# Kernel optimization log

Measured on AMD Instinct MI355X. Metric: run time of the kernel, lower is better.

## Reference

```python
import jax, jax.numpy as jnp
import numpy as np

N_NODES = 20000
DIM = 512
N_EDGES = 320000  # first N_NODES edges are self-loops so every node has a predecessor
EPS = 1e-7


def _logmap0(y):
    # Poincare ball (c=1) log map at origin: artanh(||y||) * y / ||y||
    n = jnp.linalg.norm(y, axis=-1, keepdims=True)
    nc = jnp.clip(n, EPS, 1.0 - 1e-6)
    return jnp.arctanh(nc) * y / nc


def _expmap0(v):
    # Poincare ball (c=1) exp map at origin: tanh(||v||) * v / ||v||
    n = jnp.linalg.norm(v, axis=-1, keepdims=True)
    nc = jnp.maximum(n, EPS)
    return jnp.tanh(nc) * v / nc


def setup_inputs() -> dict:
    key = jax.random.key(0)
    ks = jax.random.split(key, 9)
    x_raw = jax.random.normal(ks[0], (N_NODES, DIM), dtype=jnp.float32)
    nrm = jnp.linalg.norm(x_raw, axis=-1, keepdims=True)
    x = 0.7 * x_raw / (1.0 + nrm)  # strictly inside the unit ball

    rng = np.random.RandomState(0)
    src_rand = rng.randint(0, N_NODES, size=N_EDGES - N_NODES)
    dst_rand = rng.randint(0, N_NODES, size=N_EDGES - N_NODES)
    loop = np.arange(N_NODES)
    src = jnp.asarray(np.concatenate([loop, src_rand]), dtype=jnp.int32)
    dst = jnp.asarray(np.concatenate([loop, dst_rand]), dtype=jnp.int32)

    s = 1.0 / np.sqrt(DIM)
    Wq = jax.random.normal(ks[1], (DIM, DIM), jnp.float32) * s
    bq = jax.random.normal(ks[2], (DIM,), jnp.float32) * 0.01
    Wk = jax.random.normal(ks[3], (DIM, DIM), jnp.float32) * s
    bk = jax.random.normal(ks[4], (DIM,), jnp.float32) * 0.01
    Wv = jax.random.normal(ks[5], (DIM, DIM), jnp.float32) * s
    bv = jax.random.normal(ks[6], (DIM,), jnp.float32) * 0.01
    Wo = jax.random.normal(ks[7], (DIM, DIM), jnp.float32) * s
    bo = jax.random.normal(ks[8], (DIM,), jnp.float32) * 0.01
    return dict(x=x, src=src, dst=dst, Wq=Wq, bq=bq, Wk=Wk, bk=bk,
                Wv=Wv, bv=bv, Wo=Wo, bo=bo)


def reference(x, src, dst, Wq, bq, Wk, bk, Wv, bv, Wo, bo):
    n_nodes, d = x.shape
    scale = 1.0 / jnp.sqrt(jnp.asarray(d, x.dtype))

    t = _logmap0(x)                                  # [N, d] tangent vectors
    q = (t @ Wq.T + bq) * scale                      # torch MHA scales q
    k = t @ Wk.T + bk
    v = t @ Wv.T + bv

    # Per-destination attention over predecessor (src) neighbors.
    scores = jnp.sum(q[dst] * k[src], axis=-1)       # [E]
    m = jax.ops.segment_max(scores, dst, num_segments=n_nodes)
    e = jnp.exp(scores - m[dst])
    denom = jax.ops.segment_sum(e, dst, num_segments=n_nodes)
    alpha = e / denom[dst]                           # [E] softmax weights

    attn = jax.ops.segment_sum(alpha[:, None] * v[src], dst,
                               num_segments=n_nodes)  # [N, d]
    new_h = attn @ Wo.T + bo                          # MHA output projection
    return _expmap0(new_h)
```

## Files before the change

### kernel.cpp

```cpp
#include <hip/hip_runtime.h>
#include <math.h>
#include <stdint.h>

#define NND 20000
#define DIMK 512
#define NE  320000

typedef __attribute__((ext_vector_type(8))) short short8;
typedef __attribute__((ext_vector_type(4))) float floatx4;
typedef __attribute__((ext_vector_type(2))) float float2v;

__device__ inline float bf2f(unsigned short h) {
    unsigned int u = ((unsigned int)h) << 16;
    return __uint_as_float(u);
}
__device__ inline unsigned short f2bf(float f) {
    unsigned int u = __float_as_uint(f);
    unsigned int r = (u + 0x7fffu + ((u >> 16) & 1u)) >> 16;
    return (unsigned short)r;
}
__device__ __forceinline__ float2v up2(unsigned int u) {
    float2v r;
    r.x = __uint_as_float(u << 16);
    r.y = __uint_as_float(u & 0xFFFF0000u);
    return r;
}

__device__ __forceinline__ void gld_lds16(const unsigned short* g, unsigned short* l) {
    __builtin_amdgcn_global_load_lds(
        (const __attribute__((address_space(1))) void*)g,
        (__attribute__((address_space(3))) void*)l,
        16, 0, 0);
}

__global__ __launch_bounds__(256) void k_pre(const float* __restrict__ x,
                                             const float* __restrict__ Wq,
                                             const float* __restrict__ Wk,
                                             const float* __restrict__ Wv,
                                             const float* __restrict__ Wo,
                                             const float* __restrict__ bq,
                                             const float* __restrict__ bv,
                                             const float* __restrict__ bo,
                                             const int* __restrict__ dst,
                                             int* __restrict__ counts,
                                             unsigned short* __restrict__ t,
                                             unsigned short* __restrict__ WqTs,
                                             unsigned short* __restrict__ WkT,
                                             unsigned short* __restrict__ WvT,
                                             unsigned short* __restrict__ WoB,
                                             float* __restrict__ bh,
                                             float* __restrict__ bpr,
                                             float scf) {
    int blk = blockIdx.x, tid = threadIdx.x;
    if (blk < 5000) {
        int row = blk * 4 + (tid >> 6);
        int lane = tid & 63;
        const floatx4* xp = (const floatx4*)(x + (size_t)row * DIMK + lane * 8);
        floatx4 x0 = xp[0], x1 = xp[1];
        float ss = 0.f;
#pragma unroll
        for (int i = 0; i < 4; i++) { ss += x0[i] * x0[i]; ss += x1[i] * x1[i]; }
#pragma unroll
        for (int off = 32; off >= 1; off >>= 1) ss += __shfl_xor(ss, off, 64);
        float n  = sqrtf(ss);
        float nc = fminf(fmaxf(n, 1e-7f), 1.0f - 1e-6f);
        float fac = atanhf(nc) / nc;
        union { short8 v; unsigned short u[8]; } o;
#pragma unroll
        for (int i = 0; i < 4; i++) { o.u[i] = f2bf(fac * x0[i]); o.u[4 + i] = f2bf(fac * x1[i]); }
        *(short8*)(t + (size_t)row * DIMK + lane * 8) = o.v;
    } else if (blk < 5256) {
        int i = (blk - 5000) * 256 + tid;
        floatx4 f = *(const floatx4*)(Wo + (size_t)i * 4);
        union { unsigned long long d; unsigned short u[4]; } o;
#pragma unroll
        for (int q = 0; q < 4; q++) o.u[q] = f2bf(f[q]);
        *(unsigned long long*)(WoB + (size_t)i * 4) = o.d;
    } else if (blk < 5448) {
        int g = blk - 5256;
        int m = g >> 6, tile = g & 63;
        int tr = tile >> 3, tc = tile & 7;
        const float* srcm = (m == 0) ? Wq : (m == 1) ? Wk : Wv;
        unsigned short* dstp = (m == 0) ? WqTs : (m == 1) ? WkT : WvT;
        float sc = (m == 0) ? scf : 1.0f;
        __shared__ float tl[64][65];
#pragma unroll
        for (int i = 0; i < 16; i++) {
            int idx = i * 256 + tid; int r = idx >> 6, c = idx & 63;
            tl[c][r] = srcm[(size_t)(tr * 64 + r) * 512 + tc * 64 + c];
        }
        __syncthreads();
#pragma unroll
        for (int i = 0; i < 16; i++) {
            int idx = i * 256 + tid; int r = idx >> 6, c = idx & 63;
            dstp[(size_t)(tc * 64 + r) * 512 + tr * 64 + c] = f2bf(tl[r][c] * sc);
        }
    } else if (blk < 5450) {
        int col = (blk - 5448) * 256 + tid;
        float s = 0.f;
#pragma unroll 8
        for (int m = 0; m < 512; m++) s += bq[m] * Wk[(size_t)m * 512 + col];
        bh[col] = s * scf;
    } else if (blk < 5578) {
        int row = (blk - 5450) * 4 + (tid >> 6);
        int lane = tid & 63;
        const floatx4* wp = (const floatx4*)(Wo + (size_t)row * 512 + lane * 8);
        const floatx4* bp = (const floatx4*)(bv + lane * 8);
        floatx4 a0 = wp[0], a1 = wp[1], c0 = bp[0], c1 = bp[1];
        float s = 0.f;
#pragma unroll
        for (int i = 0; i < 4; i++) { s += a0[i] * c0[i]; s += a1[i] * c1[i]; }
#pragma unroll
        for (int off = 32; off >= 1; off >>= 1) s += __shfl_xor(s, off, 64);
        if (lane == 0) bpr[row] = s + bo[row];
    } else {
        int e = (blk - 5578) * 256 + tid;
        if (e < NE) atomicAdd(&counts[dst[e]], 1);
    }
}

__device__ __forceinline__ void gemm_tile(int vb,
                                          const unsigned short* __restrict__ A,
                                          const unsigned short* __restrict__ B,
                                          const float* __restrict__ biasf,
                                          unsigned short* __restrict__ out_q,
                                          float* __restrict__ out_f,
                                          int M, int MT, int NT, int Ncols,
                                          unsigned short* smem) {
    int xcd = vb & 7, i = vb >> 3;
    int nt = i % NT, mt = (i / NT) * 8 + xcd;
    if (mt >= MT) return;
    int m0 = mt * 128, n0 = nt * 128;
    int tid = threadIdx.x, wv = tid >> 6, ln = tid & 63;
    int lr = ln & 15, qd = ln >> 4;
    int mh = wv >> 1, nh = wv & 1;

    floatx4 acc[4][4] = {};
    int srow = wv * 16 + (ln >> 2);
    int scol = (((ln & 3) ^ (ln >> 4)) & 3) * 8;
    int fsw = (qd ^ (lr >> 2)) & 3;

    {
        unsigned short* Ab = smem;
        unsigned short* Bb = smem + 8192;
#pragma unroll
        for (int p = 0; p < 2; p++) {
            int tr = p * 64 + srow;
            int ar = m0 + tr; if (ar > M - 1) ar = M - 1;
            gld_lds16(A + (size_t)ar * DIMK + scol, Ab + (p * 64 + wv * 16) * 32);
            gld_lds16(B + (size_t)(n0 + tr) * DIMK + scol, Bb + (p * 64 + wv * 16) * 32);
        }
    }

    for (int it = 0; it < 16; it++) {
        int cur = it & 1, nxt = cur ^ 1;
        __syncthreads();
        if (it + 1 < 16) {
            int kb = (it + 1) * 32;
            unsigned short* Ab = smem + nxt * 4096;
            unsigned short* Bb = smem + 8192 + nxt * 4096;
#pragma unroll
            for (int p = 0; p < 2; p++) {
                int tr = p * 64 + srow;
                int ar = m0 + tr; if (ar > M - 1) ar = M - 1;
                gld_lds16(A + (size_t)ar * DIMK + kb + scol, Ab + (p * 64 + wv * 16) * 32);
                gld_lds16(B + (size_t)(n0 + tr) * DIMK + kb + scol, Bb + (p * 64 + wv * 16) * 32);
            }
        }
        const unsigned short* Ac = smem + cur * 4096;
        const unsigned short* Bc = smem + 8192 + cur * 4096;
        short8 af[4], bfr[4];
#pragma unroll
        for (int mi = 0; mi < 4; mi++)
            af[mi] = *(const short8*)(Ac + (mh * 64 + mi * 16 + lr) * 32 + fsw * 8);
#pragma unroll
        for (int ni = 0; ni < 4; ni++)
            bfr[ni] = *(const short8*)(Bc + (nh * 64 + ni * 16 + lr) * 32 + fsw * 8);
#pragma unroll
        for (int mi = 0; mi < 4; mi++)
#pragma unroll
            for (int ni = 0; ni < 4; ni++)
                acc[mi][ni] = __builtin_amdgcn_mfma_f32_16x16x32_bf16(af[mi], bfr[ni], acc[mi][ni], 0, 0, 0);
    }

    float bb[4];
#pragma unroll
    for (int ni = 0; ni < 4; ni++) bb[ni] = biasf[n0 + nh * 64 + ni * 16 + lr];

    if (!out_f) {
        int col0 = nt * 128;
        unsigned short* cs = smem;
#pragma unroll
        for (int g = 0; g < 4; g++) {
            __syncthreads();
            if (mh == (g >> 1)) {
                int miB = (g & 1) * 2;
#pragma unroll
                for (int m2 = 0; m2 < 2; m2++) {
                    int mi = miB + m2;
                    int lrow = mi * 16 + qd * 4 - (g & 1) * 32;
#pragma unroll
                    for (int ni = 0; ni < 4; ni++) {
                        int col = nh * 64 + ni * 16 + lr;
#pragma unroll
                        for (int r = 0; r < 4; r++)
                            cs[(lrow + r) * 128 + col] = f2bf(acc[mi][ni][r] + bb[ni]);
                    }
                }
            }
            __syncthreads();
#pragma unroll
            for (int itr = 0; itr < 2; itr++) {
                int slot = itr * 256 + tid;
                int row = slot >> 4, cg = slot & 15;
                int gm = m0 + g * 32 + row;
                if (gm < M) {
                    short8 vv = *(const short8*)(cs + row * 128 + cg * 8);
                    *(short8*)(out_q + (size_t)gm * 512 + col0 + cg * 8) = vv;
                }
            }
        }
    } else {
#pragma unroll
        for (int ni = 0; ni < 4; ni++) {
            int gn = n0 + nh * 64 + ni * 16 + lr;
#pragma unroll
            for (int mi = 0; mi < 4; mi++) {
                int gm0 = m0 + mh * 64 + mi * 16 + qd * 4;
#pragma unroll
                for (int r = 0; r < 4; r++) {
                    int gm = gm0 + r;
                    if (gm < M) out_f[(size_t)gm * Ncols + gn] = acc[mi][ni][r] + bb[ni];
                }
            }
        }
    }
}

__global__ __launch_bounds__(256) void k_scan33(const int* __restrict__ counts,
                                                int* __restrict__ offsets,
                                                int* __restrict__ pos,
                                                const unsigned short* __restrict__ WkT,
                                                const unsigned short* __restrict__ WqTs,
                                                const unsigned short* __restrict__ WoB,
                                                const unsigned short* __restrict__ WvT,
                                                unsigned short* __restrict__ Amat,
                                                unsigned short* __restrict__ Wovb) {
    __shared__ unsigned short smem[16384];
    int tid = threadIdx.x;
    if (blockIdx.x == 0) {
        const int CPT = 79;
        int base = tid * CPT;
        int tot = 0;
        for (int i = 0; i < CPT; i++) {
            int idx = base + i;
            tot += (idx < NND) ? counts[idx] : 0;
        }
        int lane = tid & 63, w = tid >> 6;
        int v = tot;
#pragma unroll
        for (int off = 1; off < 64; off <<= 1) {
            int u = __shfl_up(v, off, 64);
            if (lane >= off) v += u;
        }
        int* wsum = (int*)smem;
        if (lane == 63) wsum[w] = v;
        __syncthreads();
        int wbase = 0;
#pragma unroll
        for (int i = 0; i < 4; i++) wbase += (i < w) ? wsum[i] : 0;
        int run = wbase + (v - tot);
        for (int i = 0; i < CPT; i++) {
            int idx = base + i;
            if (idx < NND) {
                offsets[idx] = run; pos[idx] = run;
                run += counts[idx];
            }
        }
        return;
    }
    int g = blockIdx.x - 1;
    int prod = g >> 4;
    int mt = (g >> 2) & 3, nt = g & 3;
    const unsigned short* A = prod ? WoB : WkT;
    const unsigned short* B = prod ? WvT : WqTs;
    unsigned short* outp = prod ? Wovb : Amat;
    int m0 = mt * 128, n0 = nt * 128;
    int wv = tid >> 6, ln = tid & 63;
    int lr = ln & 15, qd = ln >> 4;
    int mh = wv >> 1, nh = wv & 1;
    floatx4 acc[4][4] = {};
    int srow = wv * 16 + (ln >> 2);
    int scol = (((ln & 3) ^ (ln >> 4)) & 3) * 8;
    int fsw = (qd ^ (lr >> 2)) & 3;
    {
        unsigned short* Ab = smem;
        unsigned short* Bb = smem + 8192;
#pragma unroll
        for (int p = 0; p < 2; p++) {
            int tr = p * 64 + srow;
            gld_lds16(A + (size_t)(m0 + tr) * DIMK + scol, Ab + (p * 64 + wv * 16) * 32);
            gld_lds16(B + (size_t)(n0 + tr) * DIMK + scol, Bb + (p * 64 + wv * 16) * 32);
        }
    }
    for (int it = 0; it < 16; it++) {
        int cur = it & 1, nxt = cur ^ 1;
        __syncthreads();
        if (it + 1 < 16) {
            int kb = (it + 1) * 32;
            unsigned short* Ab = smem + nxt * 4096;
            unsigned short* Bb = smem + 8192 + nxt * 4096;
#pragma unroll
            for (int p = 0; p < 2; p++) {
                int tr = p * 64 + srow;
                gld_lds16(A + (size_t)(m0 + tr) * DIMK + kb + scol, Ab + (p * 64 + wv * 16) * 32);
                gld_lds16(B + (size_t)(n0 + tr) * DIMK + kb + scol, Bb + (p * 64 + wv * 16) * 32);
            }
        }
        const unsigned short* Ac = smem + cur * 4096;
        const unsigned short* Bc = smem + 8192 + cur * 4096;
        short8 af[4], bfr[4];
#pragma unroll
        for (int mi = 0; mi < 4; mi++)
            af[mi] = *(const short8*)(Ac + (mh * 64 + mi * 16 + lr) * 32 + fsw * 8);
#pragma unroll
        for (int ni = 0; ni < 4; ni++)
            bfr[ni] = *(const short8*)(Bc + (nh * 64 + ni * 16 + lr) * 32 + fsw * 8);
#pragma unroll
        for (int mi = 0; mi < 4; mi++)
#pragma unroll
            for (int ni = 0; ni < 4; ni++)
                acc[mi][ni] = __builtin_amdgcn_mfma_f32_16x16x32_bf16(af[mi], bfr[ni], acc[mi][ni], 0, 0, 0);
    }
#pragma unroll
    for (int ni = 0; ni < 4; ni++) {
        int gn = n0 + nh * 64 + ni * 16 + lr;
#pragma unroll
        for (int mi = 0; mi < 4; mi++) {
            int gm0 = m0 + mh * 64 + mi * 16 + qd * 4;
#pragma unroll
            for (int r = 0; r < 4; r++)
                outp[(size_t)(gm0 + r) * 512 + gn] = f2bf(acc[mi][ni][r]);
        }
    }
}

__global__ __launch_bounds__(256) void k_sg(const unsigned short* __restrict__ t,
                                            const unsigned short* __restrict__ Amat,
                                            const float* __restrict__ bh,
                                            unsigned short* __restrict__ qh,
                                            const int* __restrict__ dst,
                                            const int* __restrict__ src,
                                            int* __restrict__ pos,
                                            int* __restrict__ ssrc) {
    __shared__ unsigned short smem[16384];
    int b = blockIdx.x;
    if (b < 640) {
        gemm_tile(b, t, Amat, bh, qh, nullptr, NND, 157, 4, 512, smem);
    } else {
        int e = (b - 640) * 256 + threadIdx.x;
        if (e < NE) { int p = atomicAdd(&pos[dst[e]], 1); ssrc[p] = src[e]; }
    }
}

__global__ __launch_bounds__(256) void k_proj(const unsigned short* __restrict__ A,
                                              const unsigned short* __restrict__ B,
                                              const float* __restrict__ biasf,
                                              float* __restrict__ out_f) {
    __shared__ unsigned short smem[16384];
    gemm_tile(blockIdx.x, A, B, biasf, nullptr, out_f, NND, 157, 4, 512, smem);
}

__global__ __launch_bounds__(256) void k_fsa(const int* __restrict__ offsets,
                                             const int* __restrict__ counts,
                                             const int* __restrict__ ssrc,
                                             const unsigned short* __restrict__ qb,
                                             const unsigned short* __restrict__ tb,
                                             unsigned short* __restrict__ attn) {
    __shared__ float sacc[4][32][17];
    __shared__ float sden[4];
    int n = blockIdx.x, tid = threadIdx.x;
    int wv = tid >> 6, ln = tid & 63;
    int grp = ln >> 4, li = ln & 15;
    int slot = wv * 4 + grp;
    int beg = offsets[n], end = beg + counts[n];

    const uint4* qp = (const uint4*)(qb + (size_t)n * 512 + li * 32);
    uint4 qa = qp[0], qb4 = qp[1], qc = qp[2], qd4 = qp[3];
    float2v q2[16];
    q2[0] = up2(qa.x);  q2[1] = up2(qa.y);  q2[2] = up2(qa.z);  q2[3] = up2(qa.w);
    q2[4] = up2(qb4.x); q2[5] = up2(qb4.y); q2[6] = up2(qb4.z); q2[7] = up2(qb4.w);
    q2[8] = up2(qc.x);  q2[9] = up2(qc.y);  q2[10] = up2(qc.z); q2[11] = up2(qc.w);
    q2[12] = up2(qd4.x); q2[13] = up2(qd4.y); q2[14] = up2(qd4.z); q2[15] = up2(qd4.w);

    float2v av2[16];
#pragma unroll
    for (int i = 0; i < 16; i++) av2[i] = (float2v){0.f, 0.f};
    float den = 0.f;

    for (int e = beg + slot; e < end; e += 16) {
        int row = ssrc[e];
        const uint4* tp = (const uint4*)(tb + (size_t)row * 512 + li * 32);
        uint4 ta = tp[0], tb4 = tp[1], tc = tp[2], td = tp[3];
        float2v t0 = up2(ta.x),  t1 = up2(ta.y),  t2 = up2(ta.z),  t3 = up2(ta.w);
        float2v t4 = up2(tb4.x), t5 = up2(tb4.y), t6 = up2(tb4.z), t7 = up2(tb4.w);
        float2v t8 = up2(tc.x),  t9 = up2(tc.y),  t10 = up2(tc.z), t11 = up2(tc.w);
        float2v t12 = up2(td.x), t13 = up2(td.y), t14 = up2(td.z), t15 = up2(td.w);
        float2v d2 = q2[0] * t0;
        d2 += q2[1] * t1;   d2 += q2[2] * t2;   d2 += q2[3] * t3;
        d2 += q2[4] * t4;   d2 += q2[5] * t5;   d2 += q2[6] * t6;
        d2 += q2[7] * t7;   d2 += q2[8] * t8;   d2 += q2[9] * t9;
        d2 += q2[10] * t10; d2 += q2[11] * t11; d2 += q2[12] * t12;
        d2 += q2[13] * t13; d2 += q2[14] * t14; d2 += q2[15] * t15;
        float d = d2.x + d2.y;
        d += __shfl_xor(d, 1, 64);
        d += __shfl_xor(d, 2, 64);
        d += __shfl_xor(d, 4, 64);
        d += __shfl_xor(d, 8, 64);
        float w = __expf(d);
        den += w;
        float2v w2 = {w, w};
        av2[0] += w2 * t0;   av2[1] += w2 * t1;   av2[2] += w2 * t2;
        av2[3] += w2 * t3;   av2[4] += w2 * t4;   av2[5] += w2 * t5;
        av2[6] += w2 * t6;   av2[7] += w2 * t7;   av2[8] += w2 * t8;
        av2[9] += w2 * t9;   av2[10] += w2 * t10; av2[11] += w2 * t11;
        av2[12] += w2 * t12; av2[13] += w2 * t13; av2[14] += w2 * t14;
        av2[15] += w2 * t15;
    }
#pragma unroll
    for (int off = 16; off < 64; off <<= 1) {
        den += __shfl_xor(den, off, 64);
#pragma unroll
        for (int i = 0; i < 16; i++) {
            av2[i].x += __shfl_xor(av2[i].x, off, 64);
            av2[i].y += __shfl_xor(av2[i].y, off, 64);
        }
    }
    if (grp == 0) {
#pragma unroll
        for (int i = 0; i < 16; i++) {
            sacc[wv][2 * i][li]     = av2[i].x;
            sacc[wv][2 * i + 1][li] = av2[i].y;
        }
    }
    if (ln == 0) sden[wv] = den;
    __syncthreads();
    float inv = 1.0f / (sden[0] + sden[1] + sden[2] + sden[3]);
    int c = tid * 2;
    int l0 = c >> 5, e0 = c & 31;
    float o0 = sacc[0][e0][l0] + sacc[1][e0][l0] + sacc[2][e0][l0] + sacc[3][e0][l0];
    float o1 = sacc[0][e0 + 1][l0] + sacc[1][e0 + 1][l0] + sacc[2][e0 + 1][l0] + sacc[3][e0 + 1][l0];
    attn[(size_t)n * 512 + c]     = f2bf(o0 * inv);
    attn[(size_t)n * 512 + c + 1] = f2bf(o1 * inv);
}

__global__ __launch_bounds__(64) void k_expmap(float* h) {
    int row = blockIdx.x, lane = threadIdx.x;
    floatx4* hp = (floatx4*)(h + (size_t)row * DIMK + lane * 8);
    floatx4 h0 = hp[0], h1 = hp[1];
    float ss = 0.f;
#pragma unroll
    for (int i = 0; i < 4; i++) { ss += h0[i] * h0[i]; ss += h1[i] * h1[i]; }
#pragma unroll
    for (int off = 32; off >= 1; off >>= 1) ss += __shfl_xor(ss, off, 64);
    float n  = sqrtf(ss);
    float nc = fmaxf(n, 1e-7f);
    float fac = tanhf(nc) / nc;
#pragma unroll
    for (int i = 0; i < 4; i++) { h0[i] *= fac; h1[i] *= fac; }
    hp[0] = h0; hp[1] = h1;
}

extern "C" void kernel_launch(void* const* d_in, const int* in_sizes, int n_in,
                              void* d_out, int out_size, void* d_ws, size_t ws_size,
                              hipStream_t stream) {
    const float* x  = (const float*)d_in[0];
    const int* src  = (const int*)d_in[1];
    const int* dst  = (const int*)d_in[2];
    const float* Wq = (const float*)d_in[3];
    const float* bq = (const float*)d_in[4];
    const float* Wk = (const float*)d_in[5];
    const float* Wv = (const float*)d_in[7];
    const float* bv = (const float*)d_in[8];
    const float* Wo = (const float*)d_in[9];
    const float* bo = (const float*)d_in[10];
    float* out = (float*)d_out;

    char* ws = (char*)d_ws;
    const size_t RB  = (size_t)NND * DIMK * 2;
    const size_t WB  = (size_t)DIMK * DIMK * 2;
    unsigned short* t    = (unsigned short*)(ws);
    unsigned short* qh   = (unsigned short*)(ws + RB);
    unsigned short* WqTs = (unsigned short*)(ws + 2 * RB);
    unsigned short* WkT  = (unsigned short*)(ws + 2 * RB + WB);
    unsigned short* WvT  = (unsigned short*)(ws + 2 * RB + 2 * WB);
    unsigned short* WoB  = (unsigned short*)(ws + 2 * RB + 3 * WB);
    unsigned short* Amat = (unsigned short*)(ws + 2 * RB + 4 * WB);
    unsigned short* Wovb = (unsigned short*)(ws + 2 * RB + 5 * WB);
    float* bh            = (float*)(ws + 2 * RB + 6 * WB);
    float* bpr           = (float*)(ws + 2 * RB + 6 * WB + 2048);
    char* p = ws + 2 * RB + 6 * WB + 4096;
    int* ssrc    = (int*)p;
    int* counts  = ssrc + NE;
    int* offsets = counts + NND;
    int* pos     = offsets + NND + 2;
    unsigned short* attn = qh;

    hipMemsetAsync(counts, 0, (size_t)NND * 4, stream);

    const float scf = 0.04419417382415922f;
    k_pre<<<6828, 256, 0, stream>>>(x, Wq, Wk, Wv, Wo, bq, bv, bo, dst, counts,
                                    t, WqTs, WkT, WvT, WoB, bh, bpr, scf);

    k_scan33<<<33, 256, 0, stream>>>(counts, offsets, pos,
                                     WkT, WqTs, WoB, WvT, Amat, Wovb);

    k_sg<<<640 + 1250, 256, 0, stream>>>(t, Amat, bh, qh, dst, src, pos, ssrc);

    k_fsa<<<NND, 256, 0, stream>>>(offsets, counts, ssrc, qh, t, attn);

    k_proj<<<640, 256, 0, stream>>>(attn, Wovb, bpr, out);
    k_expmap<<<NND, 64, 0, stream>>>(out);
}
```

Before: 345.9 us.

## Reuse histogram atomics for edge rank, restructure attention wavefront mapping, batch expmap rows

The counting pass now saves the atomicAdd return value as each edge's rank within its destination bucket. The scatter step can then place edges at offset plus rank with no second round of atomics, and the pos array goes away. The attention kernel now gives each wavefront whole 512-wide rows, with 8 contiguous elements per lane. It processes two edges per iteration with a full 64-lane dot-product reduction, replacing the earlier 16-lane-group layout and its costly cross-group shuffle reduction of 32 accumulators. The expmap kernel packs 4 rows into each 256-thread block to cut the number of blocks launched.

```diff
diff --git a/kernel.cpp b/kernel.cpp
--- a/kernel.cpp
+++ b/kernel.cpp
@@ -43,6 +43,7 @@
                                              const float* __restrict__ bo,
                                              const int* __restrict__ dst,
                                              int* __restrict__ counts,
+                                             int* __restrict__ rank,
                                              unsigned short* __restrict__ t,
                                              unsigned short* __restrict__ WqTs,
                                              unsigned short* __restrict__ WkT,
@@ -115,7 +116,7 @@
         if (lane == 0) bpr[row] = s + bo[row];
     } else {
         int e = (blk - 5578) * 256 + tid;
-        if (e < NE) atomicAdd(&counts[dst[e]], 1);
+        if (e < NE) rank[e] = atomicAdd(&counts[dst[e]], 1);
     }
 }
 
@@ -239,7 +240,6 @@
 
 __global__ __launch_bounds__(256) void k_scan33(const int* __restrict__ counts,
                                                 int* __restrict__ offsets,
-                                                int* __restrict__ pos,
                                                 const unsigned short* __restrict__ WkT,
                                                 const unsigned short* __restrict__ WqTs,
                                                 const unsigned short* __restrict__ WoB,
@@ -273,7 +273,7 @@
         for (int i = 0; i < CPT; i++) {
             int idx = base + i;
             if (idx < NND) {
-                offsets[idx] = run; pos[idx] = run;
+                offsets[idx] = run;
                 run += counts[idx];
             }
         }
@@ -351,7 +351,8 @@
                                             unsigned short* __restrict__ qh,
                                             const int* __restrict__ dst,
                                             const int* __restrict__ src,
-                                            int* __restrict__ pos,
+                                            const int* __restrict__ offsets,
+                                            const int* __restrict__ rank,
                                             int* __restrict__ ssrc) {
     __shared__ unsigned short smem[16384];
     int b = blockIdx.x;
@@ -359,7 +360,7 @@
         gemm_tile(b, t, Amat, bh, qh, nullptr, NND, 157, 4, 512, smem);
     } else {
         int e = (b - 640) * 256 + threadIdx.x;
-        if (e < NE) { int p = atomicAdd(&pos[dst[e]], 1); ssrc[p] = src[e]; }
+        if (e < NE) ssrc[offsets[dst[e]] + rank[e]] = src[e];
     }
 }
 
@@ -377,85 +378,65 @@
                                              const unsigned short* __restrict__ qb,
                                              const unsigned short* __restrict__ tb,
                                              unsigned short* __restrict__ attn) {
-    __shared__ float sacc[4][32][17];
+    __shared__ float sacc[4][512];
     __shared__ float sden[4];
-    int n = blockIdx.x, tid = threadIdx.x;
-    int wv = tid >> 6, ln = tid & 63;
-    int grp = ln >> 4, li = ln & 15;
-    int slot = wv * 4 + grp;
+    int n = blockIdx.x, tid = threadIdx.x, wv = tid >> 6, ln = tid & 63;
     int beg = offsets[n], end = beg + counts[n];
-
-    const uint4* qp = (const uint4*)(qb + (size_t)n * 512 + li * 32);
-    uint4 qa = qp[0], qb4 = qp[1], qc = qp[2], qd4 = qp[3];
-    float2v q2[16];
-    q2[0] = up2(qa.x);  q2[1] = up2(qa.y);  q2[2] = up2(qa.z);  q2[3] = up2(qa.w);
-    q2[4] = up2(qb4.x); q2[5] = up2(qb4.y); q2[6] = up2(qb4.z); q2[7] = up2(qb4.w);
-    q2[8] = up2(qc.x);  q2[9] = up2(qc.y);  q2[10] = up2(qc.z); q2[11] = up2(qc.w);
-    q2[12] = up2(qd4.x); q2[13] = up2(qd4.y); q2[14] = up2(qd4.z); q2[15] = up2(qd4.w);
-
-    float2v av2[16];
-#pragma unroll
-    for (int i = 0; i < 16; i++) av2[i] = (float2v){0.f, 0.f};
+    uint4 qu = *(const uint4*)(qb + (size_t)n * 512 + ln * 8);
+    float2v q0 = up2(qu.x), q1 = up2(qu.y), q2 = up2(qu.z), q3 = up2(qu.w);
+    float2v av0 = {0, 0}, av1 = {0, 0}, av2 = {0, 0}, av3 = {0, 0};
     float den = 0.f;
-
-    for (int e = beg + slot; e < end; e += 16) {
-        int row = ssrc[e];
-        const uint4* tp = (const uint4*)(tb + (size_t)row * 512 + li * 32);
-        uint4 ta = tp[0], tb4 = tp[1], tc = tp[2], td = tp[3];
-        float2v t0 = up2(ta.x),  t1 = up2(ta.y),  t2 = up2(ta.z),  t3 = up2(ta.w);
-        float2v t4 = up2(tb4.x), t5 = up2(tb4.y), t6 = up2(tb4.z), t7 = up2(tb4.w);
-        float2v t8 = up2(tc.x),  t9 = up2(tc.y),  t10 = up2(tc.z), t11 = up2(tc.w);
-        float2v t12 = up2(td.x), t13 = up2(td.y), t14 = up2(td.z), t15 = up2(td.w);
-        float2v d2 = q2[0] * t0;
-        d2 += q2[1] * t1;   d2 += q2[2] * t2;   d2 += q2[3] * t3;
-        d2 += q2[4] * t4;   d2 += q2[5] * t5;   d2 += q2[6] * t6;
-        d2 += q2[7] * t7;   d2 += q2[8] * t8;   d2 += q2[9] * t9;
-        d2 += q2[10] * t10; d2 += q2[11] * t11; d2 += q2[12] * t12;
-        d2 += q2[13] * t13; d2 += q2[14] * t14; d2 += q2[15] * t15;
-        float d = d2.x + d2.y;
-        d += __shfl_xor(d, 1, 64);
-        d += __shfl_xor(d, 2, 64);
-        d += __shfl_xor(d, 4, 64);
-        d += __shfl_xor(d, 8, 64);
-        float w = __expf(d);
-        den += w;
-        float2v w2 = {w, w};
-        av2[0] += w2 * t0;   av2[1] += w2 * t1;   av2[2] += w2 * t2;
-        av2[3] += w2 * t3;   av2[4] += w2 * t4;   av2[5] += w2 * t5;
-        av2[6] += w2 * t6;   av2[7] += w2 * t7;   av2[8] += w2 * t8;
-        av2[9] += w2 * t9;   av2[10] += w2 * t10; av2[11] += w2 * t11;
-        av2[12] += w2 * t12; av2[13] += w2 * t13; av2[14] += w2 * t14;
-        av2[15] += w2 * t15;
-    }
-#pragma unroll
-    for (int off = 16; off < 64; off <<= 1) {
-        den += __shfl_xor(den, off, 64);
-#pragma unroll
-        for (int i = 0; i < 16; i++) {
-            av2[i].x += __shfl_xor(av2[i].x, off, 64);
-            av2[i].y += __shfl_xor(av2[i].y, off, 64);
-        }
-    }
-    if (grp == 0) {
-#pragma unroll
-        for (int i = 0; i < 16; i++) {
-            sacc[wv][2 * i][li]     = av2[i].x;
-            sacc[wv][2 * i + 1][li] = av2[i].y;
-        }
-    }
+    int i = beg + wv * 2;
+    for (; i + 1 < end; i += 8) {
+        uint4 ta = *(const uint4*)(tb + (size_t)ssrc[i] * 512 + ln * 8);
+        uint4 tc = *(const uint4*)(tb + (size_t)ssrc[i + 1] * 512 + ln * 8);
+        float2v t00 = up2(ta.x), t01 = up2(ta.y), t02 = up2(ta.z), t03 = up2(ta.w);
+        float2v t10 = up2(tc.x), t11 = up2(tc.y), t12 = up2(tc.z), t13 = up2(tc.w);
+        float2v a0 = q0 * t00; a0 += q1 * t01; a0 += q2 * t02; a0 += q3 * t03;
+        float2v a1 = q0 * t10; a1 += q1 * t11; a1 += q2 * t12; a1 += q3 * t13;
+        float d0 = a0.x + a0.y, d1 = a1.x + a1.y;
+#pragma unroll
+        for (int off = 32; off >= 1; off >>= 1) {
+            d0 += __shfl_xor(d0, off, 64);
+            d1 += __shfl_xor(d1, off, 64);
+        }
+        float w0 = __expf(d0), w1 = __expf(d1);
+        den += w0 + w1;
+        float2v W0 = {w0, w0}, W1 = {w1, w1};
+        av0 += W0 * t00; av0 += W1 * t10;
+        av1 += W0 * t01; av1 += W1 * t11;
+        av2 += W0 * t02; av2 += W1 * t12;
+        av3 += W0 * t03; av3 += W1 * t13;
+    }
+    if (i < end) {
+        uint4 ta = *(const uint4*)(tb + (size_t)ssrc[i] * 512 + ln * 8);
+        float2v t00 = up2(ta.x), t01 = up2(ta.y), t02 = up2(ta.z), t03 = up2(ta.w);
+        float2v a0 = q0 * t00; a0 += q1 * t01; a0 += q2 * t02; a0 += q3 * t03;
+        float d0 = a0.x + a0.y;
+#pragma unroll
+        for (int off = 32; off >= 1; off >>= 1) d0 += __shfl_xor(d0, off, 64);
+        float w0 = __expf(d0);
+        den += w0;
+        float2v W0 = {w0, w0};
+        av0 += W0 * t00; av1 += W0 * t01; av2 += W0 * t02; av3 += W0 * t03;
+    }
+    floatx4 s0v = {av0.x, av0.y, av1.x, av1.y};
+    floatx4 s1v = {av2.x, av2.y, av3.x, av3.y};
+    *(floatx4*)&sacc[wv][ln * 8]     = s0v;
+    *(floatx4*)&sacc[wv][ln * 8 + 4] = s1v;
     if (ln == 0) sden[wv] = den;
     __syncthreads();
     float inv = 1.0f / (sden[0] + sden[1] + sden[2] + sden[3]);
     int c = tid * 2;
-    int l0 = c >> 5, e0 = c & 31;
-    float o0 = sacc[0][e0][l0] + sacc[1][e0][l0] + sacc[2][e0][l0] + sacc[3][e0][l0];
-    float o1 = sacc[0][e0 + 1][l0] + sacc[1][e0 + 1][l0] + sacc[2][e0 + 1][l0] + sacc[3][e0 + 1][l0];
+    float o0 = sacc[0][c] + sacc[1][c] + sacc[2][c] + sacc[3][c];
+    float o1 = sacc[0][c + 1] + sacc[1][c + 1] + sacc[2][c + 1] + sacc[3][c + 1];
     attn[(size_t)n * 512 + c]     = f2bf(o0 * inv);
     attn[(size_t)n * 512 + c + 1] = f2bf(o1 * inv);
 }
 
-__global__ __launch_bounds__(64) void k_expmap(float* h) {
-    int row = blockIdx.x, lane = threadIdx.x;
+__global__ __launch_bounds__(256) void k_expmap(float* h) {
+    int row = blockIdx.x * 4 + (threadIdx.x >> 6);
+    int lane = threadIdx.x & 63;
     floatx4* hp = (floatx4*)(h + (size_t)row * DIMK + lane * 8);
     floatx4 h0 = hp[0], h1 = hp[1];
     float ss = 0.f;
@@ -503,22 +484,23 @@
     int* ssrc    = (int*)p;
     int* counts  = ssrc + NE;
     int* offsets = counts + NND;
-    int* pos     = offsets + NND + 2;
+    int* rank    = offsets + NND + 2;
     unsigned short* attn = qh;
 
     hipMemsetAsync(counts, 0, (size_t)NND * 4, stream);
 
     const float scf = 0.04419417382415922f;
     k_pre<<<6828, 256, 0, stream>>>(x, Wq, Wk, Wv, Wo, bq, bv, bo, dst, counts,
-                                    t, WqTs, WkT, WvT, WoB, bh, bpr, scf);
-
-    k_scan33<<<33, 256, 0, stream>>>(counts, offsets, pos,
+                                    rank, t, WqTs, WkT, WvT, WoB, bh, bpr, scf);
+
+    k_scan33<<<33, 256, 0, stream>>>(counts, offsets,
                                      WkT, WqTs, WoB, WvT, Amat, Wovb);
 
-    k_sg<<<640 + 1250, 256, 0, stream>>>(t, Amat, bh, qh, dst, src, pos, ssrc);
+    k_sg<<<640 + 1250, 256, 0, stream>>>(t, Amat, bh, qh, dst, src,
+                                         offsets, rank, ssrc);
 
     k_fsa<<<NND, 256, 0, stream>>>(offsets, counts, ssrc, qh, t, attn);
 
     k_proj<<<640, 256, 0, stream>>>(attn, Wovb, bpr, out);
-    k_expmap<<<NND, 64, 0, stream>>>(out);
-}
+    k_expmap<<<5000, 256, 0, stream>>>(out);
+}
```

Measured after the change: 286.3 us. 1.21x faster.
